# Kernel optimization log

Measured on AMD Instinct MI355X. Metric: run time of the kernel, lower is better.

The kernel has to match this reference:

```python
import jax, jax.numpy as jnp
import numpy as np

ALPHA = 0.3
N_TAGS = 50  # POS tag vocabulary size (key space of the histogram)
B, S, R = 16, 160, 40


def setup_inputs() -> dict:
    key = jax.random.key(0)
    k1, k2, k3, k4, k5, k6 = jax.random.split(key, 6)
    return {
        "a_arc": jax.random.normal(k1, (B, S, S), dtype=jnp.float32),
        "a_rel": jax.random.normal(k2, (B, S, S, R), dtype=jnp.float32),
        "s_arc": jax.random.normal(k3, (B, S, S), dtype=jnp.float32),
        "s_rel": jax.random.normal(k4, (B, S, S, R), dtype=jnp.float32),
        "adds": jax.random.randint(k5, (B, S), 0, N_TAGS, dtype=jnp.int32),
        "pos": jax.random.randint(k6, (B, S), 0, N_TAGS, dtype=jnp.int32),
        "n_tags": N_TAGS,
    }


def reference(a_arc, a_rel, s_arc, s_rel, adds, pos, n_tags):
    # Histogram accumulation: score[(t1, t2)] += a_arc[i, p1, p2]
    # where t1 = adds[i, p1], t2 = adds[i, p2].  Flatten the pair key.
    R_ = a_rel.shape[-1]
    key_add = (adds[:, :, None] * n_tags + adds[:, None, :]).reshape(-1)  # [B*S*S]
    n_seg = n_tags * n_tags
    tab_arc = jax.ops.segment_sum(a_arc.reshape(-1), key_add, num_segments=n_seg)          # [T^2]
    tab_rel = jax.ops.segment_sum(a_rel.reshape(-1, R_), key_add, num_segments=n_seg)      # [T^2, R]
    # Gather back keyed on pos-tag pairs and blend with alpha.
    key_pos = pos[:, :, None] * n_tags + pos[:, None, :]  # [B, S, S]
    s_arc_out = s_arc + tab_arc[key_pos] * ALPHA
    s_rel_out = s_rel + tab_rel[key_pos] * ALPHA
    return s_arc_out, s_rel_out
```

## Files before the change

### kernel.cpp

```cpp
#include <hip/hip_runtime.h>

#define ALPHA 0.3f
#define NT    50
#define B_    16
#define S_    160
#define RR    40
#define Q_    (RR / 4)
#define NROW  (B_ * S_)
#define NPAIR (B_ * S_ * S_)
#define NSEG  (NT * NT)
#define NREL  (NPAIR * RR)
#define NREL4 (NPAIR * Q_)
#define NARC4 (NPAIR / 4)
#define NCOL  (NT * RR + NT)
#define CW    2052

__global__ void zero_tab(float* __restrict__ tab, int n) {
    int i = blockIdx.x * blockDim.x + threadIdx.x;
    if (i < n) tab[i] = 0.0f;
}

__global__ void build_lists(const int* __restrict__ adds,
                            int* __restrict__ colstart,
                            int* __restrict__ collist) {
    __shared__ int tags[S_];
    __shared__ int cnt[NT];
    __shared__ int start[NT + 1];
    int b   = blockIdx.x;
    int tid = threadIdx.x;
    if (tid < S_) tags[tid] = adds[b * S_ + tid];
    __syncthreads();
    if (tid < NT) {
        int c = 0;
        for (int i = 0; i < S_; i++) c += (tags[i] == tid);
        cnt[tid] = c;
    }
    __syncthreads();
    if (tid == 0) {
        int s = 0;
        for (int t = 0; t < NT; t++) { start[t] = s; s += cnt[t]; }
        start[NT] = s;
    }
    __syncthreads();
    if (tid <= NT) colstart[b * 64 + tid] = start[tid];
    if (tid < NT) {
        int slot = start[tid];
        for (int i = 0; i < S_; i++)
            if (tags[i] == tid) collist[b * S_ + slot++] = i;
    }
}

template <int TO_C>
__global__ __launch_bounds__(128) void stage1(const float* __restrict__ a_arc,
                                              const float4* __restrict__ a_rel4,
                                              const int* __restrict__ adds,
                                              const int* __restrict__ colstart,
                                              const int* __restrict__ collist,
                                              float* __restrict__ C,
                                              float* __restrict__ tab_arc,
                                              float* __restrict__ tab_rel) {
    __shared__ int s_start[NT + 1];
    __shared__ int s_list[S_];
    int row = blockIdx.x;
    int b   = row / S_;
    int tid = threadIdx.x;
    for (int i = tid; i <= NT; i += 128) s_start[i] = colstart[b * 64 + i];
    for (int i = tid; i < S_; i += 128) s_list[i] = collist[b * S_ + i];
    __syncthreads();

    const float4* arow  = a_rel4 + (size_t)row * (S_ * Q_);
    const float*  aarow = a_arc + (size_t)row * S_;
    int t1 = TO_C ? 0 : adds[row];

    for (int cell = tid; cell < NT * Q_; cell += 128) {
        int t2 = cell / Q_;
        int q  = cell - t2 * Q_;
        float4 acc = make_float4(0.f, 0.f, 0.f, 0.f);
        int e1 = s_start[t2 + 1];
        for (int e = s_start[t2]; e < e1; ++e) {
            float4 v = arow[s_list[e] * Q_ + q];
            acc.x += v.x; acc.y += v.y; acc.z += v.z; acc.w += v.w;
        }
        if (TO_C) {
            ((float4*)(C + (size_t)row * CW))[cell] = acc;
        } else {
            float* dst = tab_rel + (size_t)t1 * (NT * RR) + cell * 4;
            atomicAdd(dst + 0, acc.x); atomicAdd(dst + 1, acc.y);
            atomicAdd(dst + 2, acc.z); atomicAdd(dst + 3, acc.w);
        }
    }
    if (tid < NT) {
        float acc = 0.f;
        int e1 = s_start[tid + 1];
        for (int e = s_start[tid]; e < e1; ++e) acc += aarow[s_list[e]];
        if (TO_C) C[(size_t)row * CW + NT * RR + tid] = acc;
        else      atomicAdd(tab_arc + t1 * NT + tid, acc);
    }
}

__global__ __launch_bounds__(256) void stage2(const float* __restrict__ C,
                                              const int* __restrict__ colstart,
                                              const int* __restrict__ collist,
                                              float* __restrict__ tab_arc,
                                              float* __restrict__ tab_rel) {
    int t1 = blockIdx.y;
    int c  = blockIdx.x * 256 + threadIdx.x;
    if (c >= NCOL) return;
    float acc = 0.f;
    for (int b = 0; b < B_; b++) {
        int s0 = colstart[b * 64 + t1], s1 = colstart[b * 64 + t1 + 1];
        for (int j = s0; j < s1; j++) {
            int row = b * S_ + collist[b * S_ + j];
            acc += C[(size_t)row * CW + c];
        }
    }
    if (c < NT * RR) tab_rel[t1 * (NT * RR) + c] = acc;
    else             tab_arc[t1 * NT + (c - NT * RR)] = acc;
}

__global__ __launch_bounds__(256) void apply_flat(const float* __restrict__ s_arc,
                                                  const float4* __restrict__ s_rel4,
                                                  const int* __restrict__ pos,
                                                  const float* __restrict__ tab_arc,
                                                  const float4* __restrict__ tab_rel4,
                                                  float* __restrict__ out_arc,
                                                  float4* __restrict__ out_rel4) {
    const int nthreads = gridDim.x * blockDim.x;
    for (int t = blockIdx.x * blockDim.x + threadIdx.x;
         t < NREL4 + NARC4; t += nthreads) {
        if (t < NREL4) {
            int pair = t / Q_;
            int q    = t - pair * Q_;
            int b    = pair / (S_ * S_);
            int rem  = pair - b * (S_ * S_);
            int p1   = rem / S_;
            int p2   = rem - p1 * S_;
            int key  = pos[b * S_ + p1] * NT + pos[b * S_ + p2];
            float4 sv = s_rel4[t];
            float4 tv = tab_rel4[key * Q_ + q];
            float4 o;
            o.x = sv.x + ALPHA * tv.x;
            o.y = sv.y + ALPHA * tv.y;
            o.z = sv.z + ALPHA * tv.z;
            o.w = sv.w + ALPHA * tv.w;
            out_rel4[t] = o;
        } else {
            int j   = t - NREL4;
            int e0  = j * 4;
            int b   = e0 / (S_ * S_);
            int rem = e0 - b * (S_ * S_);
            int p1  = rem / S_;
            int p2  = rem - p1 * S_;
            const int* posb = pos + b * S_;
            int base = posb[p1] * NT;
            float4 sv = ((const float4*)s_arc)[j];
            float4 o;
            o.x = sv.x + ALPHA * tab_arc[base + posb[p2 + 0]];
            o.y = sv.y + ALPHA * tab_arc[base + posb[p2 + 1]];
            o.z = sv.z + ALPHA * tab_arc[base + posb[p2 + 2]];
            o.w = sv.w + ALPHA * tab_arc[base + posb[p2 + 3]];
            ((float4*)out_arc)[j] = o;
        }
    }
}

extern "C" void kernel_launch(void* const* d_in, const int* in_sizes, int n_in,
                              void* d_out, int out_size, void* d_ws, size_t ws_size,
                              hipStream_t stream) {
    const float*  a_arc = (const float*)d_in[0];
    const float4* a_rel = (const float4*)d_in[1];
    const float*  s_arc = (const float*)d_in[2];
    const float4* s_rel = (const float4*)d_in[3];
    const int*    adds  = (const int*)d_in[4];
    const int*    pos   = (const int*)d_in[5];

    float* tab_arc  = (float*)d_ws;
    float* tab_rel  = tab_arc + NSEG;
    int*   colstart = (int*)(tab_rel + NSEG * RR);
    int*   collist  = colstart + B_ * 64;
    float* C        = (float*)(collist + B_ * S_);
    C = (float*)(((uintptr_t)C + 15) & ~(uintptr_t)15);

    size_t need_lists = (size_t)(NSEG * (RR + 1)) * 4
                      + (size_t)(B_ * 64 + B_ * S_) * 4 + 16;
    size_t need_full  = need_lists + (size_t)NROW * CW * 4;

    float*  out_arc = (float*)d_out;
    float4* out_rel = (float4*)(out_arc + NPAIR);

    const int BLK = 256;

    build_lists<<<B_, 192, 0, stream>>>(adds, colstart, collist);

    if (ws_size >= need_full) {
        stage1<1><<<NROW, 128, 0, stream>>>(a_arc, a_rel, adds, colstart, collist,
                                            C, nullptr, nullptr);
        dim3 g2((NCOL + 255) / 256, NT);
        stage2<<<g2, 256, 0, stream>>>(C, colstart, collist, tab_arc, tab_rel);
    } else {
        int n_tab = NSEG * (RR + 1);
        zero_tab<<<(n_tab + BLK - 1) / BLK, BLK, 0, stream>>>(tab_arc, n_tab);
        stage1<0><<<NROW, 128, 0, stream>>>(a_arc, a_rel, adds, colstart, collist,
                                            nullptr, tab_arc, tab_rel);
    }

    apply_flat<<<2048, 256, 0, stream>>>(s_arc, s_rel, pos, tab_arc,
                                         (const float4*)tab_rel, out_arc, out_rel);
}
```

Baseline: 83.40 us.

## Stage a_rel rows in LDS for stage1 and unroll apply kernel with batched loads

Stage1 now copies each block's full a_rel row (about 25.6 KB) and its a_arc row into shared memory with coalesced loads before the scattered per-tag gathers, which then read from LDS instead of issuing irregular global loads. Block size goes from 128 to 256 threads. The apply kernel is split into fixed rel and arc block ranges, each thread handling 8 strided elements with four loads issued together per batch to raise memory-level parallelism. The extra LDS per block lowers occupancy, and the apply kernel hard-codes element counts that must divide exactly.

```diff
diff --git a/kernel.cpp b/kernel.cpp
--- a/kernel.cpp
+++ b/kernel.cpp
@@ -9,11 +9,15 @@
 #define NROW  (B_ * S_)
 #define NPAIR (B_ * S_ * S_)
 #define NSEG  (NT * NT)
-#define NREL  (NPAIR * RR)
 #define NREL4 (NPAIR * Q_)
 #define NARC4 (NPAIR / 4)
 #define NCOL  (NT * RR + NT)
 #define CW    2052
+
+#define REL_BLOCKS 2000
+#define REL_STRIDE (REL_BLOCKS * 256)
+#define ARC_BLOCKS 50
+#define ARC_STRIDE (ARC_BLOCKS * 256)
 
 __global__ void zero_tab(float* __restrict__ tab, int n) {
     int i = blockIdx.x * blockDim.x + threadIdx.x;
@@ -51,7 +55,7 @@
 }
 
 template <int TO_C>
-__global__ __launch_bounds__(128) void stage1(const float* __restrict__ a_arc,
+__global__ __launch_bounds__(256) void stage1(const float* __restrict__ a_arc,
                                               const float4* __restrict__ a_rel4,
                                               const int* __restrict__ adds,
                                               const int* __restrict__ colstart,
@@ -59,26 +63,36 @@
                                               float* __restrict__ C,
                                               float* __restrict__ tab_arc,
                                               float* __restrict__ tab_rel) {
-    __shared__ int s_start[NT + 1];
-    __shared__ int s_list[S_];
+    __shared__ float4 a_lds[S_ * Q_];
+    __shared__ float4 aarc_lds[S_ / 4];
+    __shared__ int    s_start[NT + 1];
+    __shared__ int    s_list[S_];
     int row = blockIdx.x;
     int b   = row / S_;
     int tid = threadIdx.x;
-    for (int i = tid; i <= NT; i += 128) s_start[i] = colstart[b * 64 + i];
-    for (int i = tid; i < S_; i += 128) s_list[i] = collist[b * S_ + i];
-    __syncthreads();
-
-    const float4* arow  = a_rel4 + (size_t)row * (S_ * Q_);
-    const float*  aarow = a_arc + (size_t)row * S_;
+
+    for (int i = tid; i <= NT; i += 256) s_start[i] = colstart[b * 64 + i];
+    for (int i = tid; i < S_; i += 256)  s_list[i]  = collist[b * S_ + i];
+
+    const float4* arow = a_rel4 + (size_t)row * (S_ * Q_);
+#pragma unroll
+    for (int k = 0; k < 7; ++k) {
+        int idx = k * 256 + tid;
+        if (idx < S_ * Q_) a_lds[idx] = arow[idx];
+    }
+    if (tid < S_ / 4)
+        aarc_lds[tid] = ((const float4*)(a_arc + (size_t)row * S_))[tid];
+    __syncthreads();
+
     int t1 = TO_C ? 0 : adds[row];
 
-    for (int cell = tid; cell < NT * Q_; cell += 128) {
+    for (int cell = tid; cell < NT * Q_; cell += 256) {
         int t2 = cell / Q_;
         int q  = cell - t2 * Q_;
         float4 acc = make_float4(0.f, 0.f, 0.f, 0.f);
         int e1 = s_start[t2 + 1];
         for (int e = s_start[t2]; e < e1; ++e) {
-            float4 v = arow[s_list[e] * Q_ + q];
+            float4 v = a_lds[s_list[e] * Q_ + q];
             acc.x += v.x; acc.y += v.y; acc.z += v.z; acc.w += v.w;
         }
         if (TO_C) {
@@ -90,9 +104,10 @@
         }
     }
     if (tid < NT) {
+        const float* aarcf = (const float*)aarc_lds;
         float acc = 0.f;
         int e1 = s_start[tid + 1];
-        for (int e = s_start[tid]; e < e1; ++e) acc += aarow[s_list[e]];
+        for (int e = s_start[tid]; e < e1; ++e) acc += aarcf[s_list[e]];
         if (TO_C) C[(size_t)row * CW + NT * RR + tid] = acc;
         else      atomicAdd(tab_arc + t1 * NT + tid, acc);
     }
@@ -118,34 +133,63 @@
     else             tab_arc[t1 * NT + (c - NT * RR)] = acc;
 }
 
-__global__ __launch_bounds__(256) void apply_flat(const float* __restrict__ s_arc,
-                                                  const float4* __restrict__ s_rel4,
-                                                  const int* __restrict__ pos,
-                                                  const float* __restrict__ tab_arc,
-                                                  const float4* __restrict__ tab_rel4,
-                                                  float* __restrict__ out_arc,
-                                                  float4* __restrict__ out_rel4) {
-    const int nthreads = gridDim.x * blockDim.x;
-    for (int t = blockIdx.x * blockDim.x + threadIdx.x;
-         t < NREL4 + NARC4; t += nthreads) {
-        if (t < NREL4) {
-            int pair = t / Q_;
-            int q    = t - pair * Q_;
-            int b    = pair / (S_ * S_);
-            int rem  = pair - b * (S_ * S_);
-            int p1   = rem / S_;
-            int p2   = rem - p1 * S_;
-            int key  = pos[b * S_ + p1] * NT + pos[b * S_ + p2];
-            float4 sv = s_rel4[t];
-            float4 tv = tab_rel4[key * Q_ + q];
-            float4 o;
-            o.x = sv.x + ALPHA * tv.x;
-            o.y = sv.y + ALPHA * tv.y;
-            o.z = sv.z + ALPHA * tv.z;
-            o.w = sv.w + ALPHA * tv.w;
-            out_rel4[t] = o;
-        } else {
-            int j   = t - NREL4;
+__device__ __forceinline__ int keyq(const int* __restrict__ pos, int t) {
+    int pair = t / Q_;
+    int q    = t - pair * Q_;
+    int b    = pair / (S_ * S_);
+    int rem  = pair - b * (S_ * S_);
+    int p1   = rem / S_;
+    int p2   = rem - p1 * S_;
+    return (pos[b * S_ + p1] * NT + pos[b * S_ + p2]) * Q_ + q;
+}
+
+__global__ __launch_bounds__(256) void apply_v2(const float* __restrict__ s_arc,
+                                                const float4* __restrict__ s_rel4,
+                                                const int* __restrict__ pos,
+                                                const float* __restrict__ tab_arc,
+                                                const float4* __restrict__ tab_rel4,
+                                                float* __restrict__ out_arc,
+                                                float4* __restrict__ out_rel4) {
+    int bid = blockIdx.x, tid = threadIdx.x;
+    if (bid < REL_BLOCKS) {
+        const int t0 = bid * 256 + tid;
+#pragma unroll
+        for (int half = 0; half < 2; ++half) {
+            const int ta = t0 + (half * 4 + 0) * REL_STRIDE;
+            const int tb = t0 + (half * 4 + 1) * REL_STRIDE;
+            const int tc = t0 + (half * 4 + 2) * REL_STRIDE;
+            const int td = t0 + (half * 4 + 3) * REL_STRIDE;
+            float4 sv0 = s_rel4[ta];
+            float4 sv1 = s_rel4[tb];
+            float4 sv2 = s_rel4[tc];
+            float4 sv3 = s_rel4[td];
+            int k0 = keyq(pos, ta);
+            int k1 = keyq(pos, tb);
+            int k2 = keyq(pos, tc);
+            int k3 = keyq(pos, td);
+            float4 tv0 = tab_rel4[k0];
+            float4 tv1 = tab_rel4[k1];
+            float4 tv2 = tab_rel4[k2];
+            float4 tv3 = tab_rel4[k3];
+            float4 o0, o1, o2, o3;
+            o0.x = sv0.x + ALPHA * tv0.x; o0.y = sv0.y + ALPHA * tv0.y;
+            o0.z = sv0.z + ALPHA * tv0.z; o0.w = sv0.w + ALPHA * tv0.w;
+            o1.x = sv1.x + ALPHA * tv1.x; o1.y = sv1.y + ALPHA * tv1.y;
+            o1.z = sv1.z + ALPHA * tv1.z; o1.w = sv1.w + ALPHA * tv1.w;
+            o2.x = sv2.x + ALPHA * tv2.x; o2.y = sv2.y + ALPHA * tv2.y;
+            o2.z = sv2.z + ALPHA * tv2.z; o2.w = sv2.w + ALPHA * tv2.w;
+            o3.x = sv3.x + ALPHA * tv3.x; o3.y = sv3.y + ALPHA * tv3.y;
+            o3.z = sv3.z + ALPHA * tv3.z; o3.w = sv3.w + ALPHA * tv3.w;
+            out_rel4[ta] = o0;
+            out_rel4[tb] = o1;
+            out_rel4[tc] = o2;
+            out_rel4[td] = o3;
+        }
+    } else {
+        const int j0 = (bid - REL_BLOCKS) * 256 + tid;
+#pragma unroll
+        for (int k = 0; k < 8; ++k) {
+            int j   = j0 + k * ARC_STRIDE;
             int e0  = j * 4;
             int b   = e0 / (S_ * S_);
             int rem = e0 - b * (S_ * S_);
@@ -193,17 +237,17 @@
     build_lists<<<B_, 192, 0, stream>>>(adds, colstart, collist);
 
     if (ws_size >= need_full) {
-        stage1<1><<<NROW, 128, 0, stream>>>(a_arc, a_rel, adds, colstart, collist,
+        stage1<1><<<NROW, 256, 0, stream>>>(a_arc, a_rel, adds, colstart, collist,
                                             C, nullptr, nullptr);
         dim3 g2((NCOL + 255) / 256, NT);
         stage2<<<g2, 256, 0, stream>>>(C, colstart, collist, tab_arc, tab_rel);
     } else {
         int n_tab = NSEG * (RR + 1);
         zero_tab<<<(n_tab + BLK - 1) / BLK, BLK, 0, stream>>>(tab_arc, n_tab);
-        stage1<0><<<NROW, 128, 0, stream>>>(a_arc, a_rel, adds, colstart, collist,
+        stage1<0><<<NROW, 256, 0, stream>>>(a_arc, a_rel, adds, colstart, collist,
                                             nullptr, tab_arc, tab_rel);
     }
 
-    apply_flat<<<2048, 256, 0, stream>>>(s_arc, s_rel, pos, tab_arc,
-                                         (const float4*)tab_rel, out_arc, out_rel);
-}
+    apply_v2<<<REL_BLOCKS + ARC_BLOCKS, 256, 0, stream>>>(
+        s_arc, s_rel, pos, tab_arc, (const float4*)tab_rel, out_arc, out_rel);
+}
```

Measured after the change: 81.72 us. 2.0% less time.
